# Performance work log

Hardware: AMD Instinct MI355X
Metric: run time of the kernel (lower is better)

Reference implementation:

```python
import jax, jax.numpy as jnp
import numpy as np

EMBED_DIM = 1024
B, S = 8, 2048


def setup_inputs() -> dict:
    key = jax.random.key(0)
    ks = jax.random.split(key, 9)
    d = EMBED_DIM
    scale = 1.0 / np.sqrt(d)
    return {
        "x": jax.random.normal(ks[0], (B, S, d), dtype=jnp.float32),
        "Wq": jax.random.normal(ks[1], (d, d), dtype=jnp.float32) * scale,
        "bq": jnp.zeros((d,), dtype=jnp.float32),
        "Wk": jax.random.normal(ks[2], (d, d), dtype=jnp.float32) * scale,
        "bk": jnp.zeros((d,), dtype=jnp.float32),
        "Wv": jax.random.normal(ks[3], (d, d), dtype=jnp.float32) * scale,
        "bv": jnp.zeros((d,), dtype=jnp.float32),
        "ln_gamma": jnp.ones((d,), dtype=jnp.float32),
        "ln_beta": jnp.zeros((d,), dtype=jnp.float32),
    }


def _layernorm(x, gamma, beta, eps=1e-5):
    mu = jnp.mean(x, axis=-1, keepdims=True)
    var = jnp.var(x, axis=-1, keepdims=True)
    return (x - mu) * jax.lax.rsqrt(var + eps) * gamma + beta


def reference(x, Wq, bq, Wk, bk, Wv, bv, ln_gamma, ln_beta):
    # Pre-LN single-head self-attention with residual.
    # Dropout is identity (eval mode) for a deterministic reference.
    residual = x
    xn = _layernorm(x, ln_gamma, ln_beta)
    Q = jnp.einsum('bsd,de->bse', xn, Wq.T) + bq  # torch Linear: x @ W^T + b
    K = jnp.einsum('bsd,de->bse', xn, Wk.T) + bk
    V = jnp.einsum('bsd,de->bse', xn, Wv.T) + bv
    scores = jnp.einsum('bqd,bkd->bqk', Q, K) / jnp.sqrt(jnp.float32(EMBED_DIM))
    attention_weights = jax.nn.softmax(scores, axis=-1)  # [B, S, S]
    attention_output = jnp.einsum('bqk,bkd->bqd', attention_weights, V)
    output = residual + attention_output
    return (output, attention_weights)
```

## Files before the change

kernel.cpp:

```cpp
#include <hip/hip_runtime.h>

#define EMBED 1024
#define SEQ 2048
#define BATCH 8

typedef __bf16 bf16;
typedef bf16 bf16x4 __attribute__((ext_vector_type(4)));
typedef bf16 bf16x8 __attribute__((ext_vector_type(8)));
typedef float f32x4 __attribute__((ext_vector_type(4)));

__device__ __forceinline__ void async_copy16(const bf16* g, bf16* l) {
  __builtin_amdgcn_global_load_lds(
      (const __attribute__((address_space(1))) unsigned int*)g,
      (__attribute__((address_space(3))) unsigned int*)l, 16, 0, 0);
}

template <int KDEPTH, int LDA, int LDB>
__device__ __forceinline__ void gemm_core(const bf16* __restrict__ Ab,
                                          const bf16* __restrict__ Bb,
                                          bf16* lds, f32x4 (&acc)[8][4]) {
  const int tid = (int)threadIdx.x;
  const int lane = tid & 63;
  const int wid = tid >> 6;
  const int wm = wid >> 2, wn = wid & 3;
  const int c = lane & 15, g = lane >> 4;
  const int sx = c & 7;
  constexpr int NT = KDEPTH / 64;

  int srow[4], scol[4];
#pragma unroll
  for (int r = 0; r < 4; ++r) {
    int idx = r * 512 + tid;
    srow[r] = idx >> 3;
    scol[r] = ((idx & 7) ^ ((idx >> 3) & 7)) * 8;
  }

  auto stage = [&](int bufsel, int t) {
    bf16* dst = lds + bufsel * 32768;
    const int k0 = t * 64;
#pragma unroll
    for (int r = 0; r < 4; ++r)
      async_copy16(Ab + (size_t)srow[r] * LDA + k0 + scol[r], dst + (r * 512 + tid) * 8);
#pragma unroll
    for (int r = 0; r < 4; ++r)
      async_copy16(Bb + (size_t)srow[r] * LDB + k0 + scol[r], dst + 16384 + (r * 512 + tid) * 8);
  };

  stage(0, 0);
  stage(1, 1);
  asm volatile("s_waitcnt vmcnt(8)" ::: "memory");
  __builtin_amdgcn_s_barrier();

  const int aoffb = (wm * 128 + c) * 64;
  const int boffb = (wn * 64 + c) * 64;

  for (int t = 0; t < NT; ++t) {
    const bf16* bufA = lds + (t & 1) * 32768;
    const bf16* bufB = bufA + 16384;
    bf16x8 bfr[4][2];
#pragma unroll
    for (int p = 0; p < 4; ++p) {
      bf16x8 afr[2][2];
#pragma unroll
      for (int mm = 0; mm < 2; ++mm)
#pragma unroll
        for (int ks = 0; ks < 2; ++ks)
          afr[mm][ks] = *reinterpret_cast<const bf16x8*>(
              bufA + aoffb + (p * 2 + mm) * 1024 + (((ks * 4 + g) ^ sx) * 8));
      if (p == 0) {
#pragma unroll
        for (int ni = 0; ni < 4; ++ni)
#pragma unroll
          for (int ks = 0; ks < 2; ++ks)
            bfr[ni][ks] = *reinterpret_cast<const bf16x8*>(
                bufB + boffb + ni * 1024 + (((ks * 4 + g) ^ sx) * 8));
      }
      __builtin_amdgcn_s_barrier();
      asm volatile("s_waitcnt lgkmcnt(0)" ::: "memory");
      __builtin_amdgcn_sched_barrier(0);
      __builtin_amdgcn_s_setprio(1);
#pragma unroll
      for (int mm = 0; mm < 2; ++mm)
#pragma unroll
        for (int ni = 0; ni < 4; ++ni)
#pragma unroll
          for (int ks = 0; ks < 2; ++ks)
            acc[p * 2 + mm][ni] = __builtin_amdgcn_mfma_f32_16x16x32_bf16(
                afr[mm][ks], bfr[ni][ks], acc[p * 2 + mm][ni], 0, 0, 0);
      __builtin_amdgcn_s_setprio(0);
      __builtin_amdgcn_sched_barrier(0);
      __builtin_amdgcn_s_barrier();
    }
    if (t + 2 < NT) {
      stage(t & 1, t + 2);
      asm volatile("s_waitcnt vmcnt(8)" ::: "memory");
    } else {
      asm volatile("s_waitcnt vmcnt(0)" ::: "memory");
    }
    __builtin_amdgcn_s_barrier();
  }
}

__global__ __launch_bounds__(256) void k_pre(const float* __restrict__ x,
                                             const float* __restrict__ gamma,
                                             const float* __restrict__ beta,
                                             const float* __restrict__ wq,
                                             const float* __restrict__ wk,
                                             const float* __restrict__ wv,
                                             bf16* __restrict__ xn,
                                             bf16* __restrict__ wall) {
  const int bid = (int)blockIdx.x;
  const int tid = (int)threadIdx.x;
  if (bid >= BATCH * SEQ) {
    int i4 = (bid - BATCH * SEQ) * 256 + tid;
    int m = i4 >> 18;
    int loc = i4 & 262143;
    const float* src = (m == 0) ? wq : (m == 1) ? wk : wv;
    float4 v = reinterpret_cast<const float4*>(src)[loc];
    bf16x4 o;
    o[0] = (bf16)v.x; o[1] = (bf16)v.y; o[2] = (bf16)v.z; o[3] = (bf16)v.w;
    reinterpret_cast<bf16x4*>(wall)[i4] = o;
    return;
  }
  const int row = bid;
  const float4 v = reinterpret_cast<const float4*>(x + (size_t)row * EMBED)[tid];
  float s = v.x + v.y + v.z + v.w;
  float q = v.x * v.x + v.y * v.y + v.z * v.z + v.w * v.w;
#pragma unroll
  for (int off = 1; off < 64; off <<= 1) {
    s += __shfl_xor(s, off);
    q += __shfl_xor(q, off);
  }
  __shared__ float ls[4], lq[4];
  int w = tid >> 6;
  if ((tid & 63) == 0) { ls[w] = s; lq[w] = q; }
  __syncthreads();
  s = ls[0] + ls[1] + ls[2] + ls[3];
  q = lq[0] + lq[1] + lq[2] + lq[3];
  float mean = s * (1.0f / EMBED);
  float var = q * (1.0f / EMBED) - mean * mean;
  float rstd = rsqrtf(var + 1e-5f);
  float4 gm = reinterpret_cast<const float4*>(gamma)[tid];
  float4 b = reinterpret_cast<const float4*>(beta)[tid];
  bf16x4 o;
  o[0] = (bf16)((v.x - mean) * rstd * gm.x + b.x);
  o[1] = (bf16)((v.y - mean) * rstd * gm.y + b.y);
  o[2] = (bf16)((v.z - mean) * rstd * gm.z + b.z);
  o[3] = (bf16)((v.w - mean) * rstd * gm.w + b.w);
  reinterpret_cast<bf16x4*>(xn + (size_t)row * EMBED)[tid] = o;
}

__global__ __launch_bounds__(512) void k_qkv256(const bf16* __restrict__ xn,
                                                const bf16* __restrict__ wall,
                                                const float* __restrict__ bq,
                                                const float* __restrict__ bk,
                                                const float* __restrict__ bv,
                                                bf16* __restrict__ qbuf,
                                                bf16* __restrict__ kbuf,
                                                bf16* __restrict__ vt) {
  extern __shared__ bf16 smem[];
  const int h = (int)blockIdx.x;
  const int xcd = h & 7, pos = h >> 3;
  const int z = pos >> 5;
  const int mtile = xcd * 8 + ((pos >> 2) & 7);
  const int ntile = pos & 3;
  const int tid = (int)threadIdx.x, lane = tid & 63, wid = tid >> 6;
  const int wm = wid >> 2, wn = wid & 3;
  const int cc = lane & 15, g = lane >> 4;
  const bf16* Ab = xn + (size_t)(mtile * 256) * EMBED;
  const bf16* Bb = wall + (size_t)z * EMBED * EMBED + (size_t)(ntile * 256) * EMBED;
  f32x4 acc[8][4];
#pragma unroll
  for (int i = 0; i < 8; ++i)
#pragma unroll
    for (int j = 0; j < 4; ++j) acc[i][j] = (f32x4){0.f, 0.f, 0.f, 0.f};
  gemm_core<EMBED, EMBED, EMBED>(Ab, Bb, smem, acc);

  const int c0 = ntile * 256 + wn * 64;
  const int r0 = mtile * 256 + wm * 128;
  if (z < 2) {
    bf16* o = z ? kbuf : qbuf;
    const float* bias = z ? bk : bq;
#pragma unroll
    for (int mi = 0; mi < 8; ++mi)
#pragma unroll
      for (int ni = 0; ni < 4; ++ni) {
        int col = c0 + ni * 16 + cc;
        float bb = bias[col];
#pragma unroll
        for (int j = 0; j < 4; ++j)
          o[(size_t)(r0 + mi * 16 + g * 4 + j) * EMBED + col] = (bf16)(acc[mi][ni][j] + bb);
      }
  } else {
#pragma unroll
    for (int mi = 0; mi < 8; ++mi) {
      int srow = r0 + mi * 16 + g * 4;
      int b = srow >> 11, sl = srow & (SEQ - 1);
#pragma unroll
      for (int ni = 0; ni < 4; ++ni) {
        int col = c0 + ni * 16 + cc;
        float bb = bv[col];
        bf16x4 pk;
#pragma unroll
        for (int j = 0; j < 4; ++j) pk[j] = (bf16)(acc[mi][ni][j] + bb);
        *reinterpret_cast<bf16x4*>(vt + (size_t)b * EMBED * SEQ + (size_t)col * SEQ + sl) = pk;
      }
    }
  }
}

__global__ __launch_bounds__(512) void k_scores256(const bf16* __restrict__ qm,
                                                   const bf16* __restrict__ km,
                                                   bf16* __restrict__ wbf,
                                                   float* __restrict__ partial) {
  extern __shared__ bf16 smem[];
  const int h = (int)blockIdx.x;
  const int bb = h & 7, pos = h >> 3;
  const int mtile = pos >> 3, ntile = pos & 7;
  const int tid = (int)threadIdx.x, lane = tid & 63, wid = tid >> 6;
  const int wm = wid >> 2, wn = wid & 3;
  const int cc = lane & 15, g = lane >> 4;
  const bf16* Ab = qm + (size_t)bb * SEQ * EMBED + (size_t)(mtile * 256) * EMBED;
  const bf16* Bb = km + (size_t)bb * SEQ * EMBED + (size_t)(ntile * 256) * EMBED;
  f32x4 acc[8][4];
#pragma unroll
  for (int i = 0; i < 8; ++i)
#pragma unroll
    for (int j = 0; j < 4; ++j) acc[i][j] = (f32x4){0.f, 0.f, 0.f, 0.f};
  gemm_core<EMBED, EMBED, EMBED>(Ab, Bb, smem, acc);

  float* red = (float*)smem;
  const int c0 = ntile * 256 + wn * 64;
#pragma unroll
  for (int mi = 0; mi < 8; ++mi) {
#pragma unroll
    for (int j = 0; j < 4; ++j) {
      int lrow = wm * 128 + mi * 16 + g * 4 + j;
      size_t grow = (size_t)bb * SEQ + mtile * 256 + lrow;
      float s = 0.f;
#pragma unroll
      for (int ni = 0; ni < 4; ++ni) {
        float e = __expf(acc[mi][ni][j] * 0.03125f);
        wbf[grow * SEQ + c0 + ni * 16 + cc] = (bf16)e;
        s += e;
      }
      s += __shfl_xor(s, 1);
      s += __shfl_xor(s, 2);
      s += __shfl_xor(s, 4);
      s += __shfl_xor(s, 8);
      if (cc == 0) red[lrow * 4 + wn] = s;
    }
  }
  __syncthreads();
  if (tid < 256) {
    float l = red[tid * 4 + 0] + red[tid * 4 + 1] + red[tid * 4 + 2] + red[tid * 4 + 3];
    partial[((size_t)bb * SEQ + mtile * 256 + tid) * 8 + ntile] = l;
  }
}

__global__ __launch_bounds__(256) void k_rowsum(const float* __restrict__ partial,
                                                float* __restrict__ rinv) {
  int row = blockIdx.x * 256 + threadIdx.x;
  const float* p = partial + (size_t)row * 8;
  float l = 0.f;
#pragma unroll
  for (int i = 0; i < 8; ++i) l += p[i];
  rinv[row] = 1.0f / l;
}

__global__ __launch_bounds__(512) void k_pv256(const bf16* __restrict__ wbf,
                                               const bf16* __restrict__ vt,
                                               const float* __restrict__ rinv,
                                               const float* __restrict__ xin,
                                               float* __restrict__ outp) {
  extern __shared__ bf16 smem[];
  const int h = (int)blockIdx.x;
  const int bb = h & 7, pos = h >> 3;
  const int mtile = pos >> 2, ntile = pos & 3;
  const int tid = (int)threadIdx.x, lane = tid & 63, wid = tid >> 6;
  const int wm = wid >> 2, wn = wid & 3;
  const int cc = lane & 15, g = lane >> 4;
  const bf16* Ab = wbf + (size_t)bb * SEQ * SEQ + (size_t)(mtile * 256) * SEQ;
  const bf16* Bb = vt + (size_t)bb * EMBED * SEQ + (size_t)(ntile * 256) * SEQ;
  f32x4 acc[8][4];
#pragma unroll
  for (int i = 0; i < 8; ++i)
#pragma unroll
    for (int j = 0; j < 4; ++j) acc[i][j] = (f32x4){0.f, 0.f, 0.f, 0.f};
  gemm_core<SEQ, SEQ, SEQ>(Ab, Bb, smem, acc);

  const int c0 = ntile * 256 + wn * 64;
#pragma unroll
  for (int mi = 0; mi < 8; ++mi) {
#pragma unroll
    for (int j = 0; j < 4; ++j) {
      size_t grow = (size_t)bb * SEQ + mtile * 256 + wm * 128 + mi * 16 + g * 4 + j;
      float ri = rinv[grow];
      size_t base = grow * EMBED;
#pragma unroll
      for (int ni = 0; ni < 4; ++ni) {
        size_t off = base + c0 + ni * 16 + cc;
        outp[off] = xin[off] + acc[mi][ni][j] * ri;
      }
    }
  }
}

__global__ __launch_bounds__(256) void k_norm_bf(const bf16* __restrict__ wbf,
                                                 const float* __restrict__ rinv,
                                                 float* __restrict__ attn) {
  size_t i8 = (size_t)blockIdx.x * 256 + threadIdx.x;
  int row = (int)(i8 >> 8);
  float ri = rinv[row];
  bf16x8 v = reinterpret_cast<const bf16x8*>(wbf)[i8];
  float4 lo, hi;
  lo.x = (float)v[0] * ri; lo.y = (float)v[1] * ri;
  lo.z = (float)v[2] * ri; lo.w = (float)v[3] * ri;
  hi.x = (float)v[4] * ri; hi.y = (float)v[5] * ri;
  hi.z = (float)v[6] * ri; hi.w = (float)v[7] * ri;
  reinterpret_cast<float4*>(attn)[i8 * 2] = lo;
  reinterpret_cast<float4*>(attn)[i8 * 2 + 1] = hi;
}

extern "C" void kernel_launch(void* const* d_in, const int* in_sizes, int n_in,
                              void* d_out, int out_size, void* d_ws, size_t ws_size,
                              hipStream_t stream) {
  const float* x = (const float*)d_in[0];
  const float* Wq = (const float*)d_in[1];
  const float* bq = (const float*)d_in[2];
  const float* Wk = (const float*)d_in[3];
  const float* bk = (const float*)d_in[4];
  const float* Wv = (const float*)d_in[5];
  const float* bv = (const float*)d_in[6];
  const float* gamma = (const float*)d_in[7];
  const float* beta = (const float*)d_in[8];

  float* out = (float*)d_out;
  float* attn = out + (size_t)BATCH * SEQ * EMBED;

  bf16* qbuf = (bf16*)d_out;
  bf16* kbuf = qbuf + (size_t)BATCH * SEQ * EMBED;

  bf16* xn = (bf16*)d_ws;
  bf16* wall = xn + (size_t)BATCH * SEQ * EMBED;
  bf16* wbf = (bf16*)d_ws;
  bf16* vt = (bf16*)d_ws + (size_t)BATCH * SEQ * SEQ;
  float* partial = (float*)((char*)d_ws + 100663296ull);
  float* rinv = (float*)((char*)d_ws + 100663296ull + 524288ull);

  hipFuncSetAttribute((const void*)k_qkv256, hipFuncAttributeMaxDynamicSharedMemorySize, 131072);
  hipFuncSetAttribute((const void*)k_scores256, hipFuncAttributeMaxDynamicSharedMemorySize, 131072);
  hipFuncSetAttribute((const void*)k_pv256, hipFuncAttributeMaxDynamicSharedMemorySize, 131072);

  k_pre<<<BATCH * SEQ + 3072, 256, 0, stream>>>(x, gamma, beta, Wq, Wk, Wv, xn, wall);
  k_qkv256<<<768, 512, 131072, stream>>>(xn, wall, bq, bk, bv, qbuf, kbuf, vt);
  k_scores256<<<512, 512, 131072, stream>>>(qbuf, kbuf, wbf, partial);
  k_rowsum<<<64, 256, 0, stream>>>(partial, rinv);
  k_pv256<<<256, 512, 131072, stream>>>(wbf, vt, rinv, x, out);
  k_norm_bf<<<16384, 256, 0, stream>>>(wbf, rinv, attn);
}
```

Measured before the change: 319.4 us.

## Double-buffer LDS-to-register fragments to overlap reads with MFMA in GEMM core

Restructures the GEMM inner loop so A fragments are ping-ponged across two register sets and loaded one sub-step ahead. The next tile's first A and B fragments are prefetched after the global stage completes. The waitcnt is relaxed to lgkmcnt(4), so MFMAs can start while the following LDS reads are still in flight. The last sub-step is peeled to issue the next global stage earlier. This raises register pressure and adds barrier complexity in exchange for hiding LDS latency.

New measurement: 307.8 us. -3.6%, faster.

```diff
diff --git a/kernel.cpp b/kernel.cpp
--- a/kernel.cpp
+++ b/kernel.cpp
@@ -54,29 +54,38 @@
   const int aoffb = (wm * 128 + c) * 64;
   const int boffb = (wn * 64 + c) * 64;
 
+  bf16x8 afr[2][2][2];
+  bf16x8 bfr[4][2];
+
+#pragma unroll
+  for (int mm = 0; mm < 2; ++mm)
+#pragma unroll
+    for (int ks = 0; ks < 2; ++ks)
+      afr[0][mm][ks] = *reinterpret_cast<const bf16x8*>(
+          lds + aoffb + mm * 1024 + (((ks * 4 + g) ^ sx) * 8));
+#pragma unroll
+  for (int ni = 0; ni < 4; ++ni)
+#pragma unroll
+    for (int ks = 0; ks < 2; ++ks)
+      bfr[ni][ks] = *reinterpret_cast<const bf16x8*>(
+          lds + 16384 + boffb + ni * 1024 + (((ks * 4 + g) ^ sx) * 8));
+  __builtin_amdgcn_sched_barrier(0);
+
   for (int t = 0; t < NT; ++t) {
-    const bf16* bufA = lds + (t & 1) * 32768;
-    const bf16* bufB = bufA + 16384;
-    bf16x8 bfr[4][2];
-#pragma unroll
-    for (int p = 0; p < 4; ++p) {
-      bf16x8 afr[2][2];
+    const bf16* cA = lds + (t & 1) * 32768;
+    const bf16* nA = lds + ((t + 1) & 1) * 32768;
+    const bf16* nB = nA + 16384;
+
+#pragma unroll
+    for (int p = 0; p < 3; ++p) {
 #pragma unroll
       for (int mm = 0; mm < 2; ++mm)
 #pragma unroll
         for (int ks = 0; ks < 2; ++ks)
-          afr[mm][ks] = *reinterpret_cast<const bf16x8*>(
-              bufA + aoffb + (p * 2 + mm) * 1024 + (((ks * 4 + g) ^ sx) * 8));
-      if (p == 0) {
-#pragma unroll
-        for (int ni = 0; ni < 4; ++ni)
-#pragma unroll
-          for (int ks = 0; ks < 2; ++ks)
-            bfr[ni][ks] = *reinterpret_cast<const bf16x8*>(
-                bufB + boffb + ni * 1024 + (((ks * 4 + g) ^ sx) * 8));
-      }
+          afr[(p + 1) & 1][mm][ks] = *reinterpret_cast<const bf16x8*>(
+              cA + aoffb + ((p + 1) * 2 + mm) * 1024 + (((ks * 4 + g) ^ sx) * 8));
       __builtin_amdgcn_s_barrier();
-      asm volatile("s_waitcnt lgkmcnt(0)" ::: "memory");
+      asm volatile("s_waitcnt lgkmcnt(4)" ::: "memory");
       __builtin_amdgcn_sched_barrier(0);
       __builtin_amdgcn_s_setprio(1);
 #pragma unroll
@@ -86,18 +95,47 @@
 #pragma unroll
           for (int ks = 0; ks < 2; ++ks)
             acc[p * 2 + mm][ni] = __builtin_amdgcn_mfma_f32_16x16x32_bf16(
-                afr[mm][ks], bfr[ni][ks], acc[p * 2 + mm][ni], 0, 0, 0);
+                afr[p & 1][mm][ks], bfr[ni][ks], acc[p * 2 + mm][ni], 0, 0, 0);
       __builtin_amdgcn_s_setprio(0);
       __builtin_amdgcn_sched_barrier(0);
       __builtin_amdgcn_s_barrier();
     }
-    if (t + 2 < NT) {
-      stage(t & 1, t + 2);
+
+    asm volatile("s_waitcnt lgkmcnt(0)" ::: "memory");
+    __builtin_amdgcn_s_barrier();
+    if (t + 2 < NT) stage(t & 1, t + 2);
+    __builtin_amdgcn_sched_barrier(0);
+    __builtin_amdgcn_s_setprio(1);
+#pragma unroll
+    for (int mm = 0; mm < 2; ++mm)
+#pragma unroll
+      for (int ni = 0; ni < 4; ++ni)
+#pragma unroll
+        for (int ks = 0; ks < 2; ++ks)
+          acc[6 + mm][ni] = __builtin_amdgcn_mfma_f32_16x16x32_bf16(
+              afr[1][mm][ks], bfr[ni][ks], acc[6 + mm][ni], 0, 0, 0);
+    __builtin_amdgcn_s_setprio(0);
+    __builtin_amdgcn_sched_barrier(0);
+    if (t + 2 < NT)
       asm volatile("s_waitcnt vmcnt(8)" ::: "memory");
-    } else {
+    else
       asm volatile("s_waitcnt vmcnt(0)" ::: "memory");
-    }
     __builtin_amdgcn_s_barrier();
+    if (t + 1 < NT) {
+#pragma unroll
+      for (int mm = 0; mm < 2; ++mm)
+#pragma unroll
+        for (int ks = 0; ks < 2; ++ks)
+          afr[0][mm][ks] = *reinterpret_cast<const bf16x8*>(
+              nA + aoffb + mm * 1024 + (((ks * 4 + g) ^ sx) * 8));
+#pragma unroll
+      for (int ni = 0; ni < 4; ++ni)
+#pragma unroll
+        for (int ks = 0; ks < 2; ++ks)
+          bfr[ni][ks] = *reinterpret_cast<const bf16x8*>(
+              nB + boffb + ni * 1024 + (((ks * 4 + g) ^ sx) * 8));
+      __builtin_amdgcn_sched_barrier(0);
+    }
   }
 }
 
```
